# Optimization experiments

Hardware: AMD Instinct MI355X
Metric: run time of the kernel (lower is better)

Reference implementation:

```python
import jax, jax.numpy as jnp
import numpy as np

H, K, D, HID, B = 8, 2048, 64, 1024, 8192
TEMP = 1.0
LN_EPS = 1e-5


def setup_inputs() -> dict:
    key = jax.random.key(0)
    ks = jax.random.split(key, 6)
    s = lambda k, shape, scale=0.02: jax.random.normal(k, shape, jnp.float32) * scale
    return dict(
        z=jax.random.normal(ks[0], (B, HID), jnp.float32),
        w1=s(ks[1], (H, HID, 2 * D)),
        b1=jnp.zeros((H, 2 * D), jnp.float32),
        w2=s(ks[2], (H, 2 * D, D)),
        b2=jnp.zeros((H, D), jnp.float32),
        ln_g=jnp.ones((H, D), jnp.float32),
        ln_b=jnp.zeros((H, D), jnp.float32),
        codebooks=jax.random.normal(ks[3], (H, K, D), jnp.float32) * 0.1,
        dec_w=s(ks[4], (H, D, HID // H)),
        dec_b=jnp.zeros((H, HID // H), jnp.float32),
    )


def reference(z, w1, b1, w2, b2, ln_g, ln_b, codebooks, dec_w, dec_b):
    sg = jax.lax.stop_gradient
    Bf = z.shape[0]
    # per-head projection MLP (all heads fused via einsum): [B,HID] -> [B,H,2D] -> [B,H,D]
    h1 = jax.nn.gelu(jnp.einsum('bi,hio->bho', z, w1) + b1, approximate=False)
    zh = jnp.einsum('bho,hod->bhd', h1, w2) + b2
    mu = zh.mean(-1, keepdims=True)
    var = zh.var(-1, keepdims=True)  # biased, as torch LayerNorm
    z_heads = (zh - mu) / jnp.sqrt(var + LN_EPS) * ln_g + ln_b  # [B,H,D]
    # squared-distance to codebooks: ||z||^2 + ||c||^2 - 2 z.c  -> [B,H,K]
    z_sq = (z_heads ** 2).sum(-1)[..., None]          # [B,H,1]
    c_sq = (codebooks ** 2).sum(-1)[None]             # [1,H,K]
    zc = jnp.einsum('bhd,hkd->bhk', z_heads, codebooks)
    dists = z_sq + c_sq - 2.0 * zc
    idx = jnp.argmin(dists, axis=-1)                  # [B,H] int
    z_q = codebooks[jnp.arange(H)[None, :], idx]      # gather -> [B,H,D]
    # per-head decoders then concat -> [B,HID]
    dec = lambda x: (jnp.einsum('bhd,hdo->bho', x, dec_w) + dec_b).reshape(Bf, -1)
    z_q_dec = dec(z_q)
    z_proj = dec(z_heads)
    z_q_st = z_proj + sg(z_q_dec - z_proj)
    commit = jnp.mean((z_proj - sg(z_q_dec)) ** 2)
    codebook_loss = jnp.mean((sg(z_proj) - z_q_dec) ** 2)
    # entropy regularizer over soft assignment probs
    probs = jax.nn.softmax(-dists * TEMP, axis=-1)    # [B,H,K]
    avg_probs = probs.mean(0)                         # [H,K]
    entropy = -(avg_probs * jnp.log(avg_probs + 1e-8)).sum(-1).mean()
    entropy_loss = 1.0 - entropy / np.float32(np.log(K))
    # orthogonality: pairwise co-occurrence deviation from independence
    p = jnp.zeros((H, K), jnp.float32).at[jnp.arange(H)[None, :], idx].add(1.0) / Bf  # [H,K]
    ortho = jnp.float32(0.0)
    cnt = 0
    for i in range(H):
        for j in range(i + 1, H):
            co = jnp.zeros((K, K), jnp.float32).at[idx[:, i], idx[:, j]].add(1.0) / (Bf + 1e-8)
            expected = p[i][:, None] * p[j][None, :]
            ortho = ortho + jnp.mean(jnp.abs(co - expected))
            cnt += 1
    ortho = ortho / cnt
    return z_q_st, idx, commit, codebook_loss, entropy_loss, ortho, sg(z_heads)
```

## Files before the change

kernel.cpp:

```cpp
#include <hip/hip_runtime.h>
#include <math.h>

#define H 8
#define KK 2048
#define DD 64
#define HIDN 1024
#define BB 8192
#define TWO_D 128
#define OO 128

#define WS_CSQ   1048576
#define WS_ZSQ   1064960
#define WS_IDX   1130496
#define WS_AVGP  1196032
#define WS_HIST  1212416
#define WS_ACC   1228800
#define WS_ZERO_BYTES ((16384 + 16384 + 4) * 4)

#define OUT_ZQ 0
#define OUT_IDX 8388608
#define OUT_COMMIT 8454144
#define OUT_CBL 8454145
#define OUT_ENT 8454146
#define OUT_ORTHO 8454147
#define OUT_ZH 8454148
#define W2P_OFF 3145728

typedef __attribute__((ext_vector_type(8))) short bf16x8;
typedef __attribute__((ext_vector_type(4))) float f32x4;

__device__ inline unsigned short bf16_rne(float x) {
    union { float f; unsigned u; } c; c.f = x;
    unsigned r = c.u + 0x7FFFu + ((c.u >> 16) & 1u);
    return (unsigned short)(r >> 16);
}
__device__ inline float bf16_f32(unsigned short h) {
    union { unsigned u; float f; } c; c.u = ((unsigned)h) << 16;
    return c.f;
}
__device__ inline void split3(float x, short* hh, short* mm, short* ll) {
    unsigned short h_ = bf16_rne(x);
    float r1 = x - bf16_f32(h_);
    unsigned short m_ = bf16_rne(r1);
    float r2 = r1 - bf16_f32(m_);
    unsigned short l_ = bf16_rne(r2);
    *hh = (short)h_; *mm = (short)m_; *ll = (short)l_;
}

__device__ inline void gload_lds16(const void* g, void* l) {
    __builtin_amdgcn_global_load_lds(
        (const __attribute__((address_space(1))) unsigned int*)g,
        (__attribute__((address_space(3))) unsigned int*)l, 16, 0, 0);
}

__global__ __launch_bounds__(256) void k_pre_w1(const float* __restrict__ w1, float* outp) {
    short* w1p = (short*)outp;
    int h = blockIdx.x >> 5, kc = blockIdx.x & 31;
    int t = threadIdx.x;
    int l = t & 63, w = t >> 6;
    int lb = l & 15, lg = l >> 4;
#pragma unroll
    for (int oi = 0; oi < 2; ++oi) {
        int ot = w + oi * 4;
        union { short e[8]; bf16x8 v; } uh, um, ul;
#pragma unroll
        for (int j = 0; j < 8; ++j) {
            float x = w1[(size_t)(h * HIDN + kc * 32 + lg * 8 + j) * TWO_D + ot * 16 + lb];
            split3(x, &uh.e[j], &um.e[j], &ul.e[j]);
        }
        size_t base = (((size_t)(h * 32 + kc) * 8 + ot) * 3) * 512 + l * 8;
        *(bf16x8*)(w1p + base) = uh.v;
        *(bf16x8*)(w1p + base + 512) = um.v;
        *(bf16x8*)(w1p + base + 1024) = ul.v;
    }
}

__global__ __launch_bounds__(256) void k_pre_w2(const float* __restrict__ w2, float* outp) {
    short* w2p = (short*)outp + W2P_OFF;
    int h = blockIdx.x;
    int t = threadIdx.x;
    int l = t & 63, w = t >> 6;
    int lb = l & 15, lg = l >> 4;
#pragma unroll
    for (int i = 0; i < 4; ++i) {
        int fr = w * 4 + i;
        int dt = fr >> 2, oc = fr & 3;
        union { short e[8]; bf16x8 v; } uh, um, ul;
#pragma unroll
        for (int j = 0; j < 8; ++j) {
            float x = w2[(size_t)(h * TWO_D + oc * 32 + lg * 8 + j) * DD + dt * 16 + lb];
            split3(x, &uh.e[j], &um.e[j], &ul.e[j]);
        }
        size_t base = (((size_t)(h * 4 + dt) * 4 + oc) * 3) * 512 + l * 8;
        *(bf16x8*)(w2p + base) = uh.v;
        *(bf16x8*)(w2p + base + 512) = um.v;
        *(bf16x8*)(w2p + base + 1024) = ul.v;
    }
}

__global__ __launch_bounds__(256) void k_pre(const float* __restrict__ cb, float* __restrict__ ws) {
    int h = blockIdx.x >> 3, kb = blockIdx.x & 7;
    int t = threadIdx.x;
    int lb = t & 15, lg = (t >> 4) & 3;
    short* stg = (short*)ws;
#pragma unroll
    for (int p = 0; p < 4; ++p) {
        int T = kb * 16 + p * 4 + (t >> 6);
        int k = T * 16 + lb;
        const float* row = cb + (size_t)(h * KK + k) * DD;
        float4 a0 = *(const float4*)(row + lg * 8);
        float4 a1 = *(const float4*)(row + lg * 8 + 4);
        float4 c0 = *(const float4*)(row + 32 + lg * 8);
        float4 c1 = *(const float4*)(row + 32 + lg * 8 + 4);
        float v0[8] = {a0.x, a0.y, a0.z, a0.w, a1.x, a1.y, a1.z, a1.w};
        float v1[8] = {c0.x, c0.y, c0.z, c0.w, c1.x, c1.y, c1.z, c1.w};
        union { short e[8]; bf16x8 v; } h0, h1;
        float s = 0.f;
#pragma unroll
        for (int j = 0; j < 8; ++j) {
            float x = v0[j];
            s = fmaf(x, x, s);
            h0.e[j] = (short)bf16_rne(x);
            float y = v1[j];
            s = fmaf(y, y, s);
            h1.e[j] = (short)bf16_rne(y);
        }
        int off = (T & 15) * 8 + (T >> 4);
        size_t base = ((size_t)(h * 128 + off)) * 1024 + (t & 63) * 8;
        *(bf16x8*)(stg + base) = h0.v;
        *(bf16x8*)(stg + base + 512) = h1.v;
        s += __shfl_xor(s, 16);
        s += __shfl_xor(s, 32);
        if (lg == 0) ws[WS_CSQ + h * KK + k] = s;
    }
}

__global__ __launch_bounds__(512, 4) void k1(const float* __restrict__ z, const float* __restrict__ b1,
                                             const float* __restrict__ b2, const float* __restrict__ lng,
                                             const float* __restrict__ lnb, float* out,
                                             float* __restrict__ ws) {
    __shared__ char SM[69632];
    int t = threadIdx.x;
    int h = blockIdx.y;
    int b0 = blockIdx.x * 128;
    int w = t >> 6, l = t & 63;
    int lb = l & 15, lg = l >> 4;

    const short* w2p = (const short*)out + W2P_OFF;
    const char* w1h = (const char*)out + (size_t)h * (32 * 24576);
    const float* zrow = z + (size_t)(b0 + w * 16 + lb) * HIDN + lg * 8;

    {
        char* lb0 = SM + (t >> 6) * 1024;
        const char* gb = w1h + t * 16;
#pragma unroll
        for (int r = 0; r < 3; ++r) gload_lds16(gb + r * 8192, lb0 + r * 8192);
#pragma unroll
        for (int r = 0; r < 3; ++r) gload_lds16(gb + 24576 + r * 8192, lb0 + 24576 + r * 8192);
    }
    float4 zA = *(const float4*)(zrow);
    float4 zB = *(const float4*)(zrow + 4);
    __syncthreads();

    f32x4 acc[8];
#pragma unroll
    for (int i = 0; i < 8; ++i) acc[i] = (f32x4){0.f, 0.f, 0.f, 0.f};

#pragma unroll
    for (int c = 0; c < 32; ++c) {
        if (c > 0) {
            if (c < 31) asm volatile("s_waitcnt vmcnt(3)" ::: "memory");
            else        asm volatile("s_waitcnt vmcnt(0)" ::: "memory");
            __builtin_amdgcn_sched_barrier(0);
            __builtin_amdgcn_s_barrier();
            __builtin_amdgcn_sched_barrier(0);
        }
        {
            float zc[8] = {zA.x, zA.y, zA.z, zA.w, zB.x, zB.y, zB.z, zB.w};
            union { short e[8]; bf16x8 v; } uh, um, ul;
#pragma unroll
            for (int j = 0; j < 8; ++j) split3(zc[j], &uh.e[j], &um.e[j], &ul.e[j]);
            bf16x8 bh = uh.v, bm = um.v, blo = ul.v;
            const char* bp = SM + (c & 1) * 24576;
#pragma unroll
            for (int ot = 0; ot < 8; ++ot) {
                const char* fb = bp + ot * 3072 + l * 16;
                bf16x8 ah = *(const bf16x8*)(fb);
                bf16x8 am = *(const bf16x8*)(fb + 1024);
                bf16x8 al = *(const bf16x8*)(fb + 2048);
                f32x4 cc = acc[ot];
                cc = __builtin_amdgcn_mfma_f32_16x16x32_bf16(ah, bh, cc, 0, 0, 0);
                cc = __builtin_amdgcn_mfma_f32_16x16x32_bf16(ah, bm, cc, 0, 0, 0);
                cc = __builtin_amdgcn_mfma_f32_16x16x32_bf16(am, bh, cc, 0, 0, 0);
                cc = __builtin_amdgcn_mfma_f32_16x16x32_bf16(ah, blo, cc, 0, 0, 0);
                cc = __builtin_amdgcn_mfma_f32_16x16x32_bf16(al, bh, cc, 0, 0, 0);
                cc = __builtin_amdgcn_mfma_f32_16x16x32_bf16(am, bm, cc, 0, 0, 0);
                acc[ot] = cc;
            }
        }
        __builtin_amdgcn_sched_barrier(0);
        __builtin_amdgcn_s_barrier();
        __builtin_amdgcn_sched_barrier(0);
        if (c < 31) {
            zA = *(const float4*)(zrow + (c + 1) * 32);
            zB = *(const float4*)(zrow + (c + 1) * 32 + 4);
        }
        if (c + 2 < 32) {
            char* lb0 = SM + (c & 1) * 24576 + (t >> 6) * 1024;
            const char* gb = w1h + (size_t)(c + 2) * 24576 + t * 16;
#pragma unroll
            for (int r = 0; r < 3; ++r) gload_lds16(gb + r * 8192, lb0 + r * 8192);
        }
    }
    __syncthreads();

    float* h1W = (float*)SM + w * (16 * 68);
    float* zhL = (float*)(SM + 34816);

    f32x4 a2[4];
#pragma unroll
    for (int i = 0; i < 4; ++i) a2[i] = (f32x4){0.f, 0.f, 0.f, 0.f};

#pragma unroll
    for (int half = 0; half < 2; ++half) {
#pragma unroll
        for (int oti = 0; oti < 4; ++oti) {
            int ot = half * 4 + oti;
#pragma unroll
            for (int r = 0; r < 4; ++r) {
                int o = ot * 16 + lg * 4 + r;
                float x = acc[ot][r] + b1[h * TWO_D + o];
                float gl = 0.5f * x * (1.0f + erff(x * 0.70710678118654752f));
                h1W[lb * 68 + (o - half * 64)] = gl;
            }
        }
        __syncthreads();
#pragma unroll
        for (int oci = 0; oci < 2; ++oci) {
            int oc = half * 2 + oci;
            const float* hr = h1W + lb * 68 + oci * 32 + lg * 8;
            union { short e[8]; bf16x8 v; } uh, um, ul;
#pragma unroll
            for (int j = 0; j < 8; ++j) split3(hr[j], &uh.e[j], &um.e[j], &ul.e[j]);
            bf16x8 bh = uh.v, bm = um.v, blo = ul.v;
#pragma unroll
            for (int dt = 0; dt < 4; ++dt) {
                const short* fb = w2p + (((size_t)(h * 4 + dt) * 4 + oc) * 3) * 512 + l * 8;
                bf16x8 ah = *(const bf16x8*)(fb);
                bf16x8 am = *(const bf16x8*)(fb + 512);
                bf16x8 al = *(const bf16x8*)(fb + 1024);
                f32x4 cc = a2[dt];
                cc = __builtin_amdgcn_mfma_f32_16x16x32_bf16(ah, bh, cc, 0, 0, 0);
                cc = __builtin_amdgcn_mfma_f32_16x16x32_bf16(ah, bm, cc, 0, 0, 0);
                cc = __builtin_amdgcn_mfma_f32_16x16x32_bf16(am, bh, cc, 0, 0, 0);
                cc = __builtin_amdgcn_mfma_f32_16x16x32_bf16(ah, blo, cc, 0, 0, 0);
                cc = __builtin_amdgcn_mfma_f32_16x16x32_bf16(al, bh, cc, 0, 0, 0);
                cc = __builtin_amdgcn_mfma_f32_16x16x32_bf16(am, bm, cc, 0, 0, 0);
                a2[dt] = cc;
            }
        }
        __syncthreads();
    }

#pragma unroll
    for (int dt = 0; dt < 4; ++dt)
#pragma unroll
        for (int r = 0; r < 4; ++r) {
            int d = dt * 16 + lg * 4 + r;
            zhL[(w * 16 + lb) * 68 + d] = a2[dt][r] + b2[h * DD + d];
        }
    __syncthreads();

    {
        int row = t >> 2, c0 = (t & 3) * 16;
        const float* zr = zhL + row * 68 + c0;
        float v[16];
#pragma unroll
        for (int j = 0; j < 16; ++j) v[j] = zr[j];
        float s = 0.f;
#pragma unroll
        for (int j = 0; j < 16; ++j) s += v[j];
        s += __shfl_xor(s, 1); s += __shfl_xor(s, 2);
        float mu = s * (1.0f / 64.0f);
        float vv = 0.f;
#pragma unroll
        for (int j = 0; j < 16; ++j) { float d = v[j] - mu; vv = fmaf(d, d, vv); }
        vv += __shfl_xor(vv, 1); vv += __shfl_xor(vv, 2);
        float rstd = 1.0f / sqrtf(vv * (1.0f / 64.0f) + 1e-5f);
        float zn[16]; float ss = 0.f;
#pragma unroll
        for (int j = 0; j < 16; ++j) {
            float x = (v[j] - mu) * rstd * lng[h * DD + c0 + j] + lnb[h * DD + c0 + j];
            zn[j] = x; ss = fmaf(x, x, ss);
        }
        ss += __shfl_xor(ss, 1); ss += __shfl_xor(ss, 2);
        int brow = b0 + row;
        if ((t & 3) == 0) ws[WS_ZSQ + brow * H + h] = ss;
#pragma unroll
        for (int q = 0; q < 4; ++q) {
            float4 sv = {zn[q * 4 + 0], zn[q * 4 + 1], zn[q * 4 + 2], zn[q * 4 + 3]};
            *(float4*)(out + OUT_ZH + (size_t)(brow * H + h) * DD + c0 + q * 4) = sv;
        }
    }
}

#define MARGIN 0.10f
__device__ inline void stage16k(const char* gsrc, short* lbuf, int t) {
    char* lb_ = (char*)lbuf + (t >> 6) * 1024;
    const char* gb = gsrc + t * 16;
    gload_lds16(gb, lb_);
}
__global__ __launch_bounds__(1024) void k2(const float* __restrict__ cb,
                                           float* __restrict__ out, float* __restrict__ ws) {
    __shared__ short bufs[3][8192];
    __shared__ float zt[32][68];
    __shared__ float redM[8][32], redS[8][32], redE[8][32];
    __shared__ int   redK[8][32];
    __shared__ float MbL[32], SbL[32];
    __shared__ float zsqL[32];

    int t = threadIdx.x;
    int h = blockIdx.y;
    int b0 = blockIdx.x * 32;
    int w = t >> 6, l = t & 63;
    int rg = w >> 3, kg = w & 7;
    int lb = l & 15, lg = l >> 4;
    int rmy = rg * 16 + lb;

    const char* stgbase = (const char*)ws + (size_t)h * 262144;

    stage16k(stgbase, bufs[0], t);
    stage16k(stgbase + 16384, bufs[1], t);
    stage16k(stgbase + 32768, bufs[2], t);
#pragma unroll
    for (int i = 0; i < 2; ++i) {
        int q = t + i * 1024;
        int r = q >> 6, d = q & 63;
        zt[r][d] = out[OUT_ZH + (size_t)((b0 + r) * H + h) * DD + d];
    }
    if (t < 32) zsqL[t] = ws[WS_ZSQ + (b0 + t) * H + h];
    __syncthreads();

    bf16x8 bh[2], blo[2];
#pragma unroll
    for (int s = 0; s < 2; ++s) {
        const float* zr = &zt[rmy][s * 32 + lg * 8];
        union { short e[8]; bf16x8 v; } uh, ul;
#pragma unroll
        for (int j = 0; j < 8; ++j) {
            float x = zr[j];
            unsigned short hb = bf16_rne(x);
            uh.e[j] = (short)hb;
            ul.e[j] = (short)bf16_rne(x - bf16_f32(hb));
        }
        bh[s] = uh.v; blo[s] = ul.v;
    }

    f32x4 acc[16];
#pragma unroll
    for (int a = 0; a < 16; ++a) acc[a] = (f32x4){0.f, 0.f, 0.f, 0.f};

#pragma unroll
    for (int c = 0; c < 16; ++c) {
        if (c > 0) {
            if (c <= 13)      asm volatile("s_waitcnt vmcnt(2)" ::: "memory");
            else if (c == 14) asm volatile("s_waitcnt vmcnt(1)" ::: "memory");
            else              asm volatile("s_waitcnt vmcnt(0)" ::: "memory");
            __builtin_amdgcn_sched_barrier(0);
            __builtin_amdgcn_s_barrier();
            __builtin_amdgcn_sched_barrier(0);
        }
        {
            const short* fb = bufs[c % 3] + kg * 1024 + l * 8;
            bf16x8 C0 = *(const bf16x8*)(fb);
            bf16x8 C1 = *(const bf16x8*)(fb + 512);
            f32x4 cc = acc[c];
            cc = __builtin_amdgcn_mfma_f32_16x16x32_bf16(bh[0], C0, cc, 0, 0, 0);
            cc = __builtin_amdgcn_mfma_f32_16x16x32_bf16(blo[0], C0, cc, 0, 0, 0);
            cc = __builtin_amdgcn_mfma_f32_16x16x32_bf16(bh[1], C1, cc, 0, 0, 0);
            cc = __builtin_amdgcn_mfma_f32_16x16x32_bf16(blo[1], C1, cc, 0, 0, 0);
            acc[c] = cc;
        }
        if (c < 15) {
            __builtin_amdgcn_sched_barrier(0);
            __builtin_amdgcn_s_barrier();
            __builtin_amdgcn_sched_barrier(0);
            if (c + 3 < 16)
                stage16k(stgbase + (size_t)(c + 3) * 16384, bufs[c % 3], t);
        }
    }

    float zsqv[4];
#pragma unroll
    for (int r = 0; r < 4; ++r) zsqv[r] = zsqL[rg * 16 + lg * 4 + r];
    float mn[4] = {3.4e38f, 3.4e38f, 3.4e38f, 3.4e38f};
#pragma unroll
    for (int ai = 0; ai < 16; ++ai) {
        float cs = ws[WS_CSQ + h * KK + kg * 256 + ai * 16 + lb];
        f32x4 a = acc[ai];
        f32x4 d;
#pragma unroll
        for (int r = 0; r < 4; ++r) {
            float dv = (zsqv[r] + cs) - 2.f * a[r];
            d[r] = dv;
            mn[r] = fminf(mn[r], dv);
        }
        acc[ai] = d;
    }
#pragma unroll
    for (int off = 1; off < 16; off <<= 1)
#pragma unroll
        for (int r = 0; r < 4; ++r) mn[r] = fminf(mn[r], __shfl_xor(mn[r], off));
    if (lb == 0)
#pragma unroll
        for (int r = 0; r < 4; ++r) redM[kg][rg * 16 + lg * 4 + r] = mn[r];
    __syncthreads();
    if (t < 32) {
        float m = redM[0][t];
#pragma unroll
        for (int g = 1; g < 8; ++g) m = fminf(m, redM[g][t]);
        MbL[t] = m;
    }
    __syncthreads();
    float Mb[4];
#pragma unroll
    for (int r = 0; r < 4; ++r) Mb[r] = MbL[rg * 16 + lg * 4 + r];

    float S[4] = {0.f, 0.f, 0.f, 0.f};
    unsigned mk0 = 0, mk1 = 0, mk2 = 0, mk3 = 0;
#pragma unroll
    for (int ai = 0; ai < 16; ++ai) {
        f32x4 d = acc[ai];
        f32x4 e;
#pragma unroll
        for (int r = 0; r < 4; ++r) {
            float dv = d[r];
            float ev = __expf(Mb[r] - dv);
            S[r] += ev;
            e[r] = ev;
            bool cand = dv <= Mb[r] + MARGIN;
            if (r == 0) mk0 |= cand ? (1u << ai) : 0u;
            if (r == 1) mk1 |= cand ? (1u << ai) : 0u;
            if (r == 2) mk2 |= cand ? (1u << ai) : 0u;
            if (r == 3) mk3 |= cand ? (1u << ai) : 0u;
        }
        acc[ai] = e;
    }
#pragma unroll
    for (int off = 1; off < 16; off <<= 1)
#pragma unroll
        for (int r = 0; r < 4; ++r) S[r] += __shfl_xor(S[r], off);
    if (lb == 0)
#pragma unroll
        for (int r = 0; r < 4; ++r) redS[kg][rg * 16 + lg * 4 + r] = S[r];

    float eB[4] = {3.4e38f, 3.4e38f, 3.4e38f, 3.4e38f};
    int kB[4] = {0x7FFFFFFF, 0x7FFFFFFF, 0x7FFFFFFF, 0x7FFFFFFF};
#pragma unroll
    for (int r = 0; r < 4; ++r) {
        unsigned m = (r == 0) ? mk0 : (r == 1) ? mk1 : (r == 2) ? mk2 : mk3;
        const float* zr0 = &zt[rg * 16 + lg * 4 + r][0];
        float eBest = 3.4e38f; int kBest = 0x7FFFFFFF;
        while (m) {
            int ai = (int)__ffs(m) - 1;
            m &= m - 1;
            int k = kg * 256 + ai * 16 + lb;
            const float4* crow = (const float4*)(cb + (size_t)(h * KK + k) * DD);
            float s = 0.f;
#pragma unroll 1
            for (int q = 0; q < 16; ++q) {
                float4 cv = crow[q];
                s = fmaf(zr0[q * 4 + 0], cv.x, s);
                s = fmaf(zr0[q * 4 + 1], cv.y, s);
                s = fmaf(zr0[q * 4 + 2], cv.z, s);
                s = fmaf(zr0[q * 4 + 3], cv.w, s);
            }
            float ex = (zsqv[r] + ws[WS_CSQ + h * KK + k]) - 2.f * s;
            if (ex < eBest || (ex == eBest && k < kBest)) { eBest = ex; kBest = k; }
        }
        eB[r] = eBest; kB[r] = kBest;
    }
#pragma unroll
    for (int off = 1; off < 16; off <<= 1)
#pragma unroll
        for (int r = 0; r < 4; ++r) {
            float oe = __shfl_xor(eB[r], off);
            int ok = __shfl_xor(kB[r], off);
            if (oe < eB[r] || (oe == eB[r] && ok < kB[r])) { eB[r] = oe; kB[r] = ok; }
        }
    if (lb == 0)
#pragma unroll
        for (int r = 0; r < 4; ++r) {
            redE[kg][rg * 16 + lg * 4 + r] = eB[r];
            redK[kg][rg * 16 + lg * 4 + r] = kB[r];
        }
    __syncthreads();
    if (t < 32) {
        float Sv = redS[0][t];
#pragma unroll
        for (int g = 1; g < 8; ++g) Sv += redS[g][t];
        SbL[t] = Sv;
        float e0 = redE[0][t]; int k0_ = redK[0][t];
#pragma unroll
        for (int g = 1; g < 8; ++g) {
            float oe = redE[g][t]; int ok = redK[g][t];
            if (oe < e0 || (oe == e0 && ok < k0_)) { e0 = oe; k0_ = ok; }
        }
        out[OUT_IDX + (b0 + t) * H + h] = (float)k0_;
        ((int*)ws)[WS_IDX + (b0 + t) * H + h] = k0_;
        atomicAdd(((unsigned*)ws) + WS_HIST + h * KK + k0_, 1u);
    }
    __syncthreads();
    float invS[4];
#pragma unroll
    for (int r = 0; r < 4; ++r) invS[r] = 1.0f / SbL[rg * 16 + lg * 4 + r];

#pragma unroll
    for (int ai = 0; ai < 16; ++ai) {
        f32x4 e = acc[ai];
        float v = e[0] * invS[0];
        v = fmaf(e[1], invS[1], v);
        v = fmaf(e[2], invS[2], v);
        v = fmaf(e[3], invS[3], v);
        v += __shfl_xor(v, 16);
        v += __shfl_xor(v, 32);
        if (lg == 0) atomicAdd(ws + WS_AVGP + h * KK + kg * 256 + ai * 16 + lb, v);
    }
}

__global__ __launch_bounds__(256, 2) void k3(const float* __restrict__ cb, const float* __restrict__ dw,
                                             const float* __restrict__ db, float* __restrict__ out,
                                             float* __restrict__ ws) {
    __shared__ float zqt[32][65];
    __shared__ float zht[32][65];
    __shared__ float dwt[64][128];
    __shared__ int idxs[32];
    __shared__ double redc[4];
    int t = threadIdx.x;
    int h = blockIdx.y;
    int b0 = blockIdx.x * 32;
    if (t < 32) idxs[t] = ((const int*)ws)[WS_IDX + (b0 + t) * H + h];
    __syncthreads();
#pragma unroll
    for (int p = 0; p < 8; ++p) {
        int q = t + 256 * p;
        int r = q >> 6, d = q & 63;
        zqt[r][d] = cb[(size_t)(h * KK + idxs[r]) * DD + d];
        zht[r][d] = out[OUT_ZH + (size_t)((b0 + r) * H + h) * DD + d];
    }
#pragma unroll
    for (int p = 0; p < 8; ++p) {
        int q = t + 256 * p;
        int r = q >> 5, c4 = q & 31;
        *(float4*)(&dwt[r][c4 * 4]) = *(const float4*)(dw + (size_t)(h * DD + r) * OO + c4 * 4);
    }
    __syncthreads();
    int rg = t >> 4, cg = t & 15;
    float aq[2][8], ap[2][8];
#pragma unroll
    for (int i = 0; i < 2; ++i)
#pragma unroll
        for (int j = 0; j < 8; ++j) { aq[i][j] = 0.f; ap[i][j] = 0.f; }
#pragma unroll 4
    for (int d = 0; d < 64; ++d) {
        float q0 = zqt[rg * 2][d], q1 = zqt[rg * 2 + 1][d];
        float p0 = zht[rg * 2][d], p1 = zht[rg * 2 + 1][d];
        float4 wa = *(const float4*)(&dwt[d][cg * 8]);
        float4 wb = *(const float4*)(&dwt[d][cg * 8 + 4]);
        float ww[8] = {wa.x, wa.y, wa.z, wa.w, wb.x, wb.y, wb.z, wb.w};
#pragma unroll
        for (int j = 0; j < 8; ++j) {
            aq[0][j] = fmaf(q0, ww[j], aq[0][j]);
            aq[1][j] = fmaf(q1, ww[j], aq[1][j]);
            ap[0][j] = fmaf(p0, ww[j], ap[0][j]);
            ap[1][j] = fmaf(p1, ww[j], ap[1][j]);
        }
    }
    float lsum = 0.f;
#pragma unroll
    for (int i = 0; i < 2; ++i) {
        float vq4[8];
#pragma unroll
        for (int j = 0; j < 8; ++j) {
            float bb = db[h * OO + cg * 8 + j];
            float vq = aq[i][j] + bb;
            float vp = ap[i][j] + bb;
            vq4[j] = vp + (vq - vp);
            float e = vp - vq;
            lsum = fmaf(e, e, lsum);
        }
        float4 s0 = {vq4[0], vq4[1], vq4[2], vq4[3]};
        float4 s1 = {vq4[4], vq4[5], vq4[6], vq4[7]};
        size_t o = (size_t)(b0 + rg * 2 + i) * HIDN + h * OO + cg * 8;
        *(float4*)(out + OUT_ZQ + o) = s0;
        *(float4*)(out + OUT_ZQ + o + 4) = s1;
    }
#pragma unroll
    for (int off = 1; off < 64; off <<= 1) lsum += __shfl_xor(lsum, off);
    if ((t & 63) == 0) redc[t >> 6] = (double)lsum;
    __syncthreads();
    if (t == 0) atomicAdd((double*)(ws + WS_ACC), redc[0] + redc[1] + redc[2] + redc[3]);
}

__global__ __launch_bounds__(256) void k6(float* __restrict__ ws) {
    __shared__ unsigned slots[16384];
    __shared__ unsigned cnts[16384];
    int t = threadIdx.x;
    int bid = blockIdx.x;
    int pi = 0, pj = 1;
    {
        int c = 0;
        for (int a = 0; a < H; ++a)
            for (int b = a + 1; b < H; ++b) { if (c == bid) { pi = a; pj = b; } ++c; }
    }
    for (int s = t; s < 16384; s += 256) { slots[s] = 0xFFFFFFFFu; cnts[s] = 0u; }
    __syncthreads();
    const int* idxi = ((const int*)ws) + WS_IDX;
    for (int b = t; b < BB; b += 256) {
        unsigned key = ((unsigned)idxi[b * H + pi] << 11) | (unsigned)idxi[b * H + pj];
        unsigned p = (key * 2654435761u) >> 18;
        while (true) {
            unsigned old = atomicCAS(&slots[p], 0xFFFFFFFFu, key);
            if (old == 0xFFFFFFFFu || old == key) { atomicAdd(&cnts[p], 1u); break; }
            p = (p + 1) & 16383u;
        }
    }
    __syncthreads();
    const unsigned* hist = ((const unsigned*)ws) + WS_HIST;
    double loc = 0.0;
    for (int s = t; s < 16384; s += 256) {
        unsigned key = slots[s];
        if (key != 0xFFFFFFFFu) {
            int ki = (int)(key >> 11), kj = (int)(key & 2047u);
            float c = (float)cnts[s] * (1.0f / 8192.0f);
            float piv = (float)hist[pi * KK + ki] * (1.0f / 8192.0f);
            float pjv = (float)hist[pj * KK + kj] * (1.0f / 8192.0f);
            float e = piv * pjv;
            loc += (double)fabsf(c - e) - (double)e;
        }
    }
    double spi = 0.0, spj = 0.0;
    for (int k = t; k < KK; k += 256) {
        spi += (double)hist[pi * KK + k];
        spj += (double)hist[pj * KK + k];
    }
#pragma unroll
    for (int off = 1; off < 64; off <<= 1) {
        loc += __shfl_xor(loc, off);
        spi += __shfl_xor(spi, off);
        spj += __shfl_xor(spj, off);
    }
    __syncthreads();
    double* sc = (double*)cnts;
    if ((t & 63) == 0) { int w = t >> 6; sc[w] = loc; sc[4 + w] = spi; sc[8 + w] = spj; }
    __syncthreads();
    if (t == 0) {
        double L = sc[0] + sc[1] + sc[2] + sc[3];
        double SPI = (sc[4] + sc[5] + sc[6] + sc[7]) / 8192.0;
        double SPJ = (sc[8] + sc[9] + sc[10] + sc[11]) / 8192.0;
        atomicAdd(((double*)(ws + WS_ACC)) + 1, L + SPI * SPJ);
    }
}

__global__ __launch_bounds__(256) void k4(float* __restrict__ out, float* __restrict__ ws) {
    __shared__ double red[256];
    int t = threadIdx.x;
    double tot = 0.0;
    for (int h = 0; h < H; ++h) {
        double s = 0.0;
        for (int k = t; k < KK; k += 256) {
            double a = (double)ws[WS_AVGP + h * KK + k] / 8192.0;
            s += a * log(a + 1e-8);
        }
        tot += s;
    }
    red[t] = tot;
    __syncthreads();
    for (int off = 128; off; off >>= 1) {
        if (t < off) red[t] += red[t + off];
        __syncthreads();
    }
    if (t == 0) {
        double entropy = -red[0] / 8.0;
        out[OUT_ENT] = (float)(1.0 - entropy / log(2048.0));
        double ca = *(const double*)(ws + WS_ACC);
        float cm = (float)(ca / (8192.0 * 1024.0));
        out[OUT_COMMIT] = cm;
        out[OUT_CBL] = cm;
        double oa = *(((const double*)(ws + WS_ACC)) + 1);
        out[OUT_ORTHO] = (float)(oa / (28.0 * 4194304.0));
    }
}

extern "C" void kernel_launch(void* const* d_in, const int* in_sizes, int n_in,
                              void* d_out, int out_size, void* d_ws, size_t ws_size,
                              hipStream_t stream) {
    (void)in_sizes; (void)n_in; (void)out_size; (void)ws_size;
    const float* z   = (const float*)d_in[0];
    const float* w1  = (const float*)d_in[1];
    const float* b1  = (const float*)d_in[2];
    const float* w2  = (const float*)d_in[3];
    const float* b2  = (const float*)d_in[4];
    const float* lng = (const float*)d_in[5];
    const float* lnb = (const float*)d_in[6];
    const float* cb  = (const float*)d_in[7];
    const float* dw  = (const float*)d_in[8];
    const float* db  = (const float*)d_in[9];
    float* out = (float*)d_out;
    float* ws = (float*)d_ws;

    hipMemsetAsync(ws + WS_AVGP, 0, WS_ZERO_BYTES, stream);
    k_pre_w1<<<256, 256, 0, stream>>>(w1, out);
    k_pre_w2<<<8, 256, 0, stream>>>(w2, out);
    k_pre<<<64, 256, 0, stream>>>(cb, ws);
    k1<<<dim3(64, 8), 512, 0, stream>>>(z, b1, b2, lng, lnb, out, ws);
    k2<<<dim3(256, 8), 1024, 0, stream>>>(cb, out, ws);
    k3<<<dim3(256, 8), 256, 0, stream>>>(cb, dw, db, out, ws);
    k6<<<28, 256, 0, stream>>>(ws);
    k4<<<1, 256, 0, stream>>>(out, ws);
}
```

Baseline: 515.2 us.

## Retile projection kernel to 32x64 wave tiles and merge preprocessing launches

Projection kernel k1 now runs 1024-thread blocks covering 256 batch rows. Each wave computes a 32-row by 64-column tile, so every LDS-loaded w1 fragment feeds two MFMA row tiles instead of one. The GELU/w2 stage is split between wave pairs, and the w1 staging loads are repartitioned across 16 waves with adjusted vmcnt waits. The three weight/codebook preprocessing kernels are merged into one launch to cut launch overhead. Risks: half as many blocks and larger blocks lower occupancy and latency hiding, and a stray extra initial LDS load makes the wait counts harder to reason about.

```diff
diff --git a/kernel.cpp b/kernel.cpp
--- a/kernel.cpp
+++ b/kernel.cpp
@@ -53,221 +53,259 @@
         (__attribute__((address_space(3))) unsigned int*)l, 16, 0, 0);
 }
 
-__global__ __launch_bounds__(256) void k_pre_w1(const float* __restrict__ w1, float* outp) {
-    short* w1p = (short*)outp;
-    int h = blockIdx.x >> 5, kc = blockIdx.x & 31;
+__global__ __launch_bounds__(256) void k_pre_all(const float* __restrict__ w1, const float* __restrict__ w2,
+                                                 const float* __restrict__ cb, float* outp,
+                                                 float* __restrict__ ws) {
+    int bid = blockIdx.x;
     int t = threadIdx.x;
     int l = t & 63, w = t >> 6;
     int lb = l & 15, lg = l >> 4;
-#pragma unroll
-    for (int oi = 0; oi < 2; ++oi) {
-        int ot = w + oi * 4;
-        union { short e[8]; bf16x8 v; } uh, um, ul;
-#pragma unroll
-        for (int j = 0; j < 8; ++j) {
-            float x = w1[(size_t)(h * HIDN + kc * 32 + lg * 8 + j) * TWO_D + ot * 16 + lb];
-            split3(x, &uh.e[j], &um.e[j], &ul.e[j]);
-        }
-        size_t base = (((size_t)(h * 32 + kc) * 8 + ot) * 3) * 512 + l * 8;
-        *(bf16x8*)(w1p + base) = uh.v;
-        *(bf16x8*)(w1p + base + 512) = um.v;
-        *(bf16x8*)(w1p + base + 1024) = ul.v;
-    }
-}
-
-__global__ __launch_bounds__(256) void k_pre_w2(const float* __restrict__ w2, float* outp) {
-    short* w2p = (short*)outp + W2P_OFF;
-    int h = blockIdx.x;
-    int t = threadIdx.x;
-    int l = t & 63, w = t >> 6;
-    int lb = l & 15, lg = l >> 4;
-#pragma unroll
-    for (int i = 0; i < 4; ++i) {
-        int fr = w * 4 + i;
-        int dt = fr >> 2, oc = fr & 3;
-        union { short e[8]; bf16x8 v; } uh, um, ul;
-#pragma unroll
-        for (int j = 0; j < 8; ++j) {
-            float x = w2[(size_t)(h * TWO_D + oc * 32 + lg * 8 + j) * DD + dt * 16 + lb];
-            split3(x, &uh.e[j], &um.e[j], &ul.e[j]);
-        }
-        size_t base = (((size_t)(h * 4 + dt) * 4 + oc) * 3) * 512 + l * 8;
-        *(bf16x8*)(w2p + base) = uh.v;
-        *(bf16x8*)(w2p + base + 512) = um.v;
-        *(bf16x8*)(w2p + base + 1024) = ul.v;
-    }
-}
-
-__global__ __launch_bounds__(256) void k_pre(const float* __restrict__ cb, float* __restrict__ ws) {
-    int h = blockIdx.x >> 3, kb = blockIdx.x & 7;
-    int t = threadIdx.x;
-    int lb = t & 15, lg = (t >> 4) & 3;
-    short* stg = (short*)ws;
-#pragma unroll
-    for (int p = 0; p < 4; ++p) {
-        int T = kb * 16 + p * 4 + (t >> 6);
-        int k = T * 16 + lb;
-        const float* row = cb + (size_t)(h * KK + k) * DD;
-        float4 a0 = *(const float4*)(row + lg * 8);
-        float4 a1 = *(const float4*)(row + lg * 8 + 4);
-        float4 c0 = *(const float4*)(row + 32 + lg * 8);
-        float4 c1 = *(const float4*)(row + 32 + lg * 8 + 4);
-        float v0[8] = {a0.x, a0.y, a0.z, a0.w, a1.x, a1.y, a1.z, a1.w};
-        float v1[8] = {c0.x, c0.y, c0.z, c0.w, c1.x, c1.y, c1.z, c1.w};
-        union { short e[8]; bf16x8 v; } h0, h1;
-        float s = 0.f;
-#pragma unroll
-        for (int j = 0; j < 8; ++j) {
-            float x = v0[j];
-            s = fmaf(x, x, s);
-            h0.e[j] = (short)bf16_rne(x);
-            float y = v1[j];
-            s = fmaf(y, y, s);
-            h1.e[j] = (short)bf16_rne(y);
-        }
-        int off = (T & 15) * 8 + (T >> 4);
-        size_t base = ((size_t)(h * 128 + off)) * 1024 + (t & 63) * 8;
-        *(bf16x8*)(stg + base) = h0.v;
-        *(bf16x8*)(stg + base + 512) = h1.v;
-        s += __shfl_xor(s, 16);
-        s += __shfl_xor(s, 32);
-        if (lg == 0) ws[WS_CSQ + h * KK + k] = s;
-    }
-}
-
-__global__ __launch_bounds__(512, 4) void k1(const float* __restrict__ z, const float* __restrict__ b1,
-                                             const float* __restrict__ b2, const float* __restrict__ lng,
-                                             const float* __restrict__ lnb, float* out,
-                                             float* __restrict__ ws) {
+    if (bid < 256) {
+        short* w1p = (short*)outp;
+        int h = bid >> 5, kc = bid & 31;
+#pragma unroll
+        for (int oi = 0; oi < 2; ++oi) {
+            int ot = w + oi * 4;
+            union { short e[8]; bf16x8 v; } uh, um, ul;
+#pragma unroll
+            for (int j = 0; j < 8; ++j) {
+                float x = w1[(size_t)(h * HIDN + kc * 32 + lg * 8 + j) * TWO_D + ot * 16 + lb];
+                split3(x, &uh.e[j], &um.e[j], &ul.e[j]);
+            }
+            size_t base = (((size_t)(h * 32 + kc) * 8 + ot) * 3) * 512 + l * 8;
+            *(bf16x8*)(w1p + base) = uh.v;
+            *(bf16x8*)(w1p + base + 512) = um.v;
+            *(bf16x8*)(w1p + base + 1024) = ul.v;
+        }
+    } else if (bid < 264) {
+        short* w2p = (short*)outp + W2P_OFF;
+        int h = bid - 256;
+#pragma unroll
+        for (int i = 0; i < 4; ++i) {
+            int fr = w * 4 + i;
+            int dt = fr >> 2, oc = fr & 3;
+            union { short e[8]; bf16x8 v; } uh, um, ul;
+#pragma unroll
+            for (int j = 0; j < 8; ++j) {
+                float x = w2[(size_t)(h * TWO_D + oc * 32 + lg * 8 + j) * DD + dt * 16 + lb];
+                split3(x, &uh.e[j], &um.e[j], &ul.e[j]);
+            }
+            size_t base = (((size_t)(h * 4 + dt) * 4 + oc) * 3) * 512 + l * 8;
+            *(bf16x8*)(w2p + base) = uh.v;
+            *(bf16x8*)(w2p + base + 512) = um.v;
+            *(bf16x8*)(w2p + base + 1024) = ul.v;
+        }
+    } else {
+        int pb = bid - 264;
+        int h = pb >> 3, kb = pb & 7;
+        short* stg = (short*)ws;
+#pragma unroll
+        for (int p = 0; p < 4; ++p) {
+            int T = kb * 16 + p * 4 + (t >> 6);
+            int k = T * 16 + lb;
+            const float* row = cb + (size_t)(h * KK + k) * DD;
+            float4 a0 = *(const float4*)(row + ((t >> 4) & 3) * 8);
+            float4 a1 = *(const float4*)(row + ((t >> 4) & 3) * 8 + 4);
+            float4 c0 = *(const float4*)(row + 32 + ((t >> 4) & 3) * 8);
+            float4 c1 = *(const float4*)(row + 32 + ((t >> 4) & 3) * 8 + 4);
+            float v0[8] = {a0.x, a0.y, a0.z, a0.w, a1.x, a1.y, a1.z, a1.w};
+            float v1[8] = {c0.x, c0.y, c0.z, c0.w, c1.x, c1.y, c1.z, c1.w};
+            union { short e[8]; bf16x8 v; } h0, h1;
+            float s = 0.f;
+#pragma unroll
+            for (int j = 0; j < 8; ++j) {
+                float x = v0[j];
+                s = fmaf(x, x, s);
+                h0.e[j] = (short)bf16_rne(x);
+                float y = v1[j];
+                s = fmaf(y, y, s);
+                h1.e[j] = (short)bf16_rne(y);
+            }
+            int off = (T & 15) * 8 + (T >> 4);
+            size_t base = ((size_t)(h * 128 + off)) * 1024 + (t & 63) * 8;
+            *(bf16x8*)(stg + base) = h0.v;
+            *(bf16x8*)(stg + base + 512) = h1.v;
+            s += __shfl_xor(s, 16);
+            s += __shfl_xor(s, 32);
+            if (((t >> 4) & 3) == 0) ws[WS_CSQ + h * KK + k] = s;
+        }
+    }
+}
+
+__global__ __launch_bounds__(1024) void k1(const float* __restrict__ z, const float* __restrict__ b1,
+                                           const float* __restrict__ b2, const float* __restrict__ lng,
+                                           const float* __restrict__ lnb, float* out,
+                                           float* __restrict__ ws) {
     __shared__ char SM[69632];
     int t = threadIdx.x;
     int h = blockIdx.y;
-    int b0 = blockIdx.x * 128;
+    int b0 = blockIdx.x * 256;
     int w = t >> 6, l = t & 63;
+    int rg = w >> 1, wc = w & 1;
     int lb = l & 15, lg = l >> 4;
 
     const short* w2p = (const short*)out + W2P_OFF;
     const char* w1h = (const char*)out + (size_t)h * (32 * 24576);
-    const float* zrow = z + (size_t)(b0 + w * 16 + lb) * HIDN + lg * 8;
+    const float* zrow0 = z + (size_t)(b0 + rg * 32 + lb) * HIDN + lg * 8;
+    const float* zrow1 = zrow0 + 16 * HIDN;
 
     {
-        char* lb0 = SM + (t >> 6) * 1024;
-        const char* gb = w1h + t * 16;
-#pragma unroll
-        for (int r = 0; r < 3; ++r) gload_lds16(gb + r * 8192, lb0 + r * 8192);
-#pragma unroll
-        for (int r = 0; r < 3; ++r) gload_lds16(gb + 24576 + r * 8192, lb0 + 24576 + r * 8192);
-    }
-    float4 zA = *(const float4*)(zrow);
-    float4 zB = *(const float4*)(zrow + 4);
-    __syncthreads();
-
-    f32x4 acc[8];
-#pragma unroll
-    for (int i = 0; i < 8; ++i) acc[i] = (f32x4){0.f, 0.f, 0.f, 0.f};
+        char* d0 = SM + (t >> 6) * 1024;
+        const char* gb = w1h;
+        gload_lds16(gb + t * 16, d0 + l * 16 - l * 16 + (l * 16));
+    }
+    {
+        char* buf0 = SM;
+        char* buf1 = SM + 24576;
+        const char* g0 = w1h;
+        const char* g1 = w1h + 24576;
+        gload_lds16(g0 + t * 16, buf0 + (t >> 6) * 1024);
+        if (w < 8) gload_lds16(g0 + 16384 + t * 16, buf0 + 16384 + (t >> 6) * 1024);
+        gload_lds16(g1 + t * 16, buf1 + (t >> 6) * 1024);
+        if (w < 8) gload_lds16(g1 + 16384 + t * 16, buf1 + 16384 + (t >> 6) * 1024);
+    }
+    float4 zA0 = *(const float4*)(zrow0);
+    float4 zB0 = *(const float4*)(zrow0 + 4);
+    float4 zA1 = *(const float4*)(zrow1);
+    float4 zB1 = *(const float4*)(zrow1 + 4);
+    __syncthreads();
+
+    f32x4 acc[2][4];
+#pragma unroll
+    for (int i = 0; i < 2; ++i)
+#pragma unroll
+        for (int j = 0; j < 4; ++j) acc[i][j] = (f32x4){0.f, 0.f, 0.f, 0.f};
 
 #pragma unroll
     for (int c = 0; c < 32; ++c) {
         if (c > 0) {
-            if (c < 31) asm volatile("s_waitcnt vmcnt(3)" ::: "memory");
-            else        asm volatile("s_waitcnt vmcnt(0)" ::: "memory");
+            if (c < 31) {
+                if (w < 8) asm volatile("s_waitcnt vmcnt(2)" ::: "memory");
+                else       asm volatile("s_waitcnt vmcnt(1)" ::: "memory");
+            } else {
+                asm volatile("s_waitcnt vmcnt(0)" ::: "memory");
+            }
             __builtin_amdgcn_sched_barrier(0);
             __builtin_amdgcn_s_barrier();
             __builtin_amdgcn_sched_barrier(0);
         }
         {
-            float zc[8] = {zA.x, zA.y, zA.z, zA.w, zB.x, zB.y, zB.z, zB.w};
-            union { short e[8]; bf16x8 v; } uh, um, ul;
-#pragma unroll
-            for (int j = 0; j < 8; ++j) split3(zc[j], &uh.e[j], &um.e[j], &ul.e[j]);
-            bf16x8 bh = uh.v, bm = um.v, blo = ul.v;
+            bf16x8 bh[2], bm[2], bl[2];
+#pragma unroll
+            for (int mf = 0; mf < 2; ++mf) {
+                float zc[8];
+                if (mf == 0) { zc[0]=zA0.x; zc[1]=zA0.y; zc[2]=zA0.z; zc[3]=zA0.w; zc[4]=zB0.x; zc[5]=zB0.y; zc[6]=zB0.z; zc[7]=zB0.w; }
+                else         { zc[0]=zA1.x; zc[1]=zA1.y; zc[2]=zA1.z; zc[3]=zA1.w; zc[4]=zB1.x; zc[5]=zB1.y; zc[6]=zB1.z; zc[7]=zB1.w; }
+                union { short e[8]; bf16x8 v; } uh, um, ul;
+#pragma unroll
+                for (int j = 0; j < 8; ++j) split3(zc[j], &uh.e[j], &um.e[j], &ul.e[j]);
+                bh[mf] = uh.v; bm[mf] = um.v; bl[mf] = ul.v;
+            }
             const char* bp = SM + (c & 1) * 24576;
 #pragma unroll
-            for (int ot = 0; ot < 8; ++ot) {
-                const char* fb = bp + ot * 3072 + l * 16;
+            for (int ot = 0; ot < 4; ++ot) {
+                const char* fb = bp + (wc * 4 + ot) * 3072 + l * 16;
                 bf16x8 ah = *(const bf16x8*)(fb);
                 bf16x8 am = *(const bf16x8*)(fb + 1024);
                 bf16x8 al = *(const bf16x8*)(fb + 2048);
-                f32x4 cc = acc[ot];
-                cc = __builtin_amdgcn_mfma_f32_16x16x32_bf16(ah, bh, cc, 0, 0, 0);
-                cc = __builtin_amdgcn_mfma_f32_16x16x32_bf16(ah, bm, cc, 0, 0, 0);
-                cc = __builtin_amdgcn_mfma_f32_16x16x32_bf16(am, bh, cc, 0, 0, 0);
-                cc = __builtin_amdgcn_mfma_f32_16x16x32_bf16(ah, blo, cc, 0, 0, 0);
-                cc = __builtin_amdgcn_mfma_f32_16x16x32_bf16(al, bh, cc, 0, 0, 0);
-                cc = __builtin_amdgcn_mfma_f32_16x16x32_bf16(am, bm, cc, 0, 0, 0);
-                acc[ot] = cc;
+#pragma unroll
+                for (int mf = 0; mf < 2; ++mf) {
+                    f32x4 cc = acc[mf][ot];
+                    cc = __builtin_amdgcn_mfma_f32_16x16x32_bf16(ah, bh[mf], cc, 0, 0, 0);
+                    cc = __builtin_amdgcn_mfma_f32_16x16x32_bf16(ah, bm[mf], cc, 0, 0, 0);
+                    cc = __builtin_amdgcn_mfma_f32_16x16x32_bf16(am, bh[mf], cc, 0, 0, 0);
+                    cc = __builtin_amdgcn_mfma_f32_16x16x32_bf16(ah, bl[mf], cc, 0, 0, 0);
+                    cc = __builtin_amdgcn_mfma_f32_16x16x32_bf16(al, bh[mf], cc, 0, 0, 0);
+                    cc = __builtin_amdgcn_mfma_f32_16x16x32_bf16(am, bm[mf], cc, 0, 0, 0);
+                    acc[mf][ot] = cc;
+                }
             }
         }
         __builtin_amdgcn_sched_barrier(0);
         __builtin_amdgcn_s_barrier();
         __builtin_amdgcn_sched_barrier(0);
         if (c < 31) {
-            zA = *(const float4*)(zrow + (c + 1) * 32);
-            zB = *(const float4*)(zrow + (c + 1) * 32 + 4);
+            zA0 = *(const float4*)(zrow0 + (c + 1) * 32);
+            zB0 = *(const float4*)(zrow0 + (c + 1) * 32 + 4);
+            zA1 = *(const float4*)(zrow1 + (c + 1) * 32);
+            zB1 = *(const float4*)(zrow1 + (c + 1) * 32 + 4);
         }
         if (c + 2 < 32) {
-            char* lb0 = SM + (c & 1) * 24576 + (t >> 6) * 1024;
-            const char* gb = w1h + (size_t)(c + 2) * 24576 + t * 16;
-#pragma unroll
-            for (int r = 0; r < 3; ++r) gload_lds16(gb + r * 8192, lb0 + r * 8192);
-        }
-    }
-    __syncthreads();
-
-    float* h1W = (float*)SM + w * (16 * 68);
-    float* zhL = (float*)(SM + 34816);
-
-    f32x4 a2[4];
-#pragma unroll
-    for (int i = 0; i < 4; ++i) a2[i] = (f32x4){0.f, 0.f, 0.f, 0.f};
+            char* buf = SM + (c & 1) * 24576;
+            const char* gb = w1h + (size_t)(c + 2) * 24576;
+            gload_lds16(gb + t * 16, buf + (t >> 6) * 1024);
+            if (w < 8) gload_lds16(gb + 16384 + t * 16, buf + 16384 + (t >> 6) * 1024);
+        }
+    }
+    __syncthreads();
+
+    float* h1H = (float*)SM;
+
+    f32x4 a2[2][2];
+#pragma unroll
+    for (int i = 0; i < 2; ++i)
+#pragma unroll
+        for (int j = 0; j < 2; ++j) a2[i][j] = (f32x4){0.f, 0.f, 0.f, 0.f};
 
 #pragma unroll
     for (int half = 0; half < 2; ++half) {
-#pragma unroll
-        for (int oti = 0; oti < 4; ++oti) {
-            int ot = half * 4 + oti;
-#pragma unroll
-            for (int r = 0; r < 4; ++r) {
-                int o = ot * 16 + lg * 4 + r;
-                float x = acc[ot][r] + b1[h * TWO_D + o];
-                float gl = 0.5f * x * (1.0f + erff(x * 0.70710678118654752f));
-                h1W[lb * 68 + (o - half * 64)] = gl;
-            }
+        __syncthreads();
+        if (wc == half) {
+#pragma unroll
+            for (int ot = 0; ot < 4; ++ot)
+#pragma unroll
+                for (int mf = 0; mf < 2; ++mf)
+#pragma unroll
+                    for (int r = 0; r < 4; ++r) {
+                        int og = half * 64 + ot * 16 + lg * 4 + r;
+                        float x = acc[mf][ot][r] + b1[h * TWO_D + og];
+                        float gl = 0.5f * x * (1.0f + erff(x * 0.70710678118654752f));
+                        h1H[(rg * 32 + mf * 16 + lb) * 68 + ot * 16 + lg * 4 + r] = gl;
+                    }
         }
         __syncthreads();
 #pragma unroll
         for (int oci = 0; oci < 2; ++oci) {
             int oc = half * 2 + oci;
-            const float* hr = h1W + lb * 68 + oci * 32 + lg * 8;
-            union { short e[8]; bf16x8 v; } uh, um, ul;
-#pragma unroll
-            for (int j = 0; j < 8; ++j) split3(hr[j], &uh.e[j], &um.e[j], &ul.e[j]);
-            bf16x8 bh = uh.v, bm = um.v, blo = ul.v;
-#pragma unroll
-            for (int dt = 0; dt < 4; ++dt) {
-                const short* fb = w2p + (((size_t)(h * 4 + dt) * 4 + oc) * 3) * 512 + l * 8;
-                bf16x8 ah = *(const bf16x8*)(fb);
-                bf16x8 am = *(const bf16x8*)(fb + 512);
-                bf16x8 al = *(const bf16x8*)(fb + 1024);
-                f32x4 cc = a2[dt];
-                cc = __builtin_amdgcn_mfma_f32_16x16x32_bf16(ah, bh, cc, 0, 0, 0);
-                cc = __builtin_amdgcn_mfma_f32_16x16x32_bf16(ah, bm, cc, 0, 0, 0);
-                cc = __builtin_amdgcn_mfma_f32_16x16x32_bf16(am, bh, cc, 0, 0, 0);
-                cc = __builtin_amdgcn_mfma_f32_16x16x32_bf16(ah, blo, cc, 0, 0, 0);
-                cc = __builtin_amdgcn_mfma_f32_16x16x32_bf16(al, bh, cc, 0, 0, 0);
-                cc = __builtin_amdgcn_mfma_f32_16x16x32_bf16(am, bm, cc, 0, 0, 0);
-                a2[dt] = cc;
-            }
-        }
-        __syncthreads();
-    }
-
-#pragma unroll
-    for (int dt = 0; dt < 4; ++dt)
-#pragma unroll
-        for (int r = 0; r < 4; ++r) {
-            int d = dt * 16 + lg * 4 + r;
-            zhL[(w * 16 + lb) * 68 + d] = a2[dt][r] + b2[h * DD + d];
+#pragma unroll
+            for (int mf = 0; mf < 2; ++mf) {
+                const float* hr = h1H + (rg * 32 + mf * 16 + lb) * 68 + oci * 32 + lg * 8;
+                union { short e[8]; bf16x8 v; } uh, um, ul;
+#pragma unroll
+                for (int j = 0; j < 8; ++j) split3(hr[j], &uh.e[j], &um.e[j], &ul.e[j]);
+                bf16x8 bh = uh.v, bm = um.v, blo = ul.v;
+#pragma unroll
+                for (int dti = 0; dti < 2; ++dti) {
+                    int dt = wc * 2 + dti;
+                    const short* fb = w2p + (((size_t)(h * 4 + dt) * 4 + oc) * 3) * 512 + l * 8;
+                    bf16x8 ah = *(const bf16x8*)(fb);
+                    bf16x8 am = *(const bf16x8*)(fb + 512);
+                    bf16x8 al = *(const bf16x8*)(fb + 1024);
+                    f32x4 cc = a2[mf][dti];
+                    cc = __builtin_amdgcn_mfma_f32_16x16x32_bf16(ah, bh, cc, 0, 0, 0);
+                    cc = __builtin_amdgcn_mfma_f32_16x16x32_bf16(ah, bm, cc, 0, 0, 0);
+                    cc = __builtin_amdgcn_mfma_f32_16x16x32_bf16(am, bh, cc, 0, 0, 0);
+                    cc = __builtin_amdgcn_mfma_f32_16x16x32_bf16(ah, blo, cc, 0, 0, 0);
+                    cc = __builtin_amdgcn_mfma_f32_16x16x32_bf16(al, bh, cc, 0, 0, 0);
+                    cc = __builtin_amdgcn_mfma_f32_16x16x32_bf16(am, bm, cc, 0, 0, 0);
+                    a2[mf][dti] = cc;
+                }
+            }
+        }
+    }
+    __syncthreads();
+
+    float* zhL = (float*)SM;
+#pragma unroll
+    for (int mf = 0; mf < 2; ++mf)
+#pragma unroll
+        for (int dti = 0; dti < 2; ++dti) {
+            int dt = wc * 2 + dti;
+#pragma unroll
+            for (int r = 0; r < 4; ++r) {
+                int d = dt * 16 + lg * 4 + r;
+                zhL[(rg * 32 + mf * 16 + lb) * 68 + d] = a2[mf][dti][r] + b2[h * DD + d];
+            }
         }
     __syncthreads();
 
@@ -710,10 +748,8 @@
     float* ws = (float*)d_ws;
 
     hipMemsetAsync(ws + WS_AVGP, 0, WS_ZERO_BYTES, stream);
-    k_pre_w1<<<256, 256, 0, stream>>>(w1, out);
-    k_pre_w2<<<8, 256, 0, stream>>>(w2, out);
-    k_pre<<<64, 256, 0, stream>>>(cb, ws);
-    k1<<<dim3(64, 8), 512, 0, stream>>>(z, b1, b2, lng, lnb, out, ws);
+    k_pre_all<<<328, 256, 0, stream>>>(w1, w2, cb, out, ws);
+    k1<<<dim3(32, 8), 1024, 0, stream>>>(z, b1, b2, lng, lnb, out, ws);
     k2<<<dim3(256, 8), 1024, 0, stream>>>(cb, out, ws);
     k3<<<dim3(256, 8), 256, 0, stream>>>(cb, dw, db, out, ws);
     k6<<<28, 256, 0, stream>>>(ws);
```

Result: slower. 588.2 us (+14.2%).
